# Performance work log

Measured on AMD Instinct MI355X. Metric: run time of the kernel, lower is better.

## Reference

```python
import jax, jax.numpy as jnp
import numpy as np

NM, ND = 50000, 50000          # mirna / disease node counts
DM, DD = 256, 256              # m_sim / d_sim feature dims
F = 64                         # feature_attn_size
E = 1600000                    # number of edges (avg degree 16)
N = NM + ND
SLOPE = 0.2                    # leaky_relu negative slope


def setup_inputs() -> dict:
    key = jax.random.key(0)
    k1, k2, k3, k4, k5, k6 = jax.random.split(key, 6)
    return {
        "m_sim": jax.random.normal(k1, (NM, DM), dtype=jnp.float32),
        "d_sim": jax.random.normal(k2, (ND, DD), dtype=jnp.float32),
        "Wm": jax.random.normal(k3, (F, DM), dtype=jnp.float32) / np.sqrt(DM).astype(np.float32),
        "Wd": jax.random.normal(k4, (F, DD), dtype=jnp.float32) / np.sqrt(DD).astype(np.float32),
        "src": jax.random.randint(k5, (E,), 0, N),
        "dst": jax.random.randint(k6, (E,), 0, N),
    }


def reference(m_sim, d_sim, Wm, Wd, src, dst):
    # node projection (dropout omitted: eval mode). mirna nodes first, then disease nodes.
    z = jnp.concatenate([m_sim @ Wm.T, d_sim @ Wd.T], axis=0)  # [N, F]

    # edge attention score: dot(z_src, z_dst) then leaky_relu
    z_src = z[src]                                             # [E, F] gather
    e = jnp.sum(z_src * z[dst], axis=1)                        # [E]
    e = jax.nn.leaky_relu(e, SLOPE)

    # segment softmax over incoming edges of each dst node (numerically stable)
    emax = jax.ops.segment_max(e, dst, num_segments=N)         # [N]
    emax = jnp.where(jnp.isfinite(emax), emax, 0.0)            # isolated nodes
    ex = jnp.exp(e - emax[dst])                                # [E]
    denom = jax.ops.segment_sum(ex, dst, num_segments=N)       # [N]
    alpha = ex / denom[dst]                                    # [E]

    # weighted aggregation + elu (isolated nodes get h=0, elu(0)=0)
    h = jax.ops.segment_sum(alpha[:, None] * z_src, dst, num_segments=N)  # [N, F]
    return jax.nn.elu(h)
```

## Files before the change

### kernel.cpp

```cpp
#include <hip/hip_runtime.h>
#include <math.h>

#define NM 50000
#define ND 50000
#define NN 100000
#define DK 256
#define F  64
#define SLOPE 0.2f

#define NBZ   782
#define NPROJ (NBZ * 2)

#define NBUCK 391
#define BCAP  8192
#define CH    4096

typedef short bf16x8 __attribute__((ext_vector_type(8)));
typedef float f32x4  __attribute__((ext_vector_type(4)));

__device__ __forceinline__ void gload_lds16(const void* g, void* l) {
    __builtin_amdgcn_global_load_lds((const __attribute__((address_space(1))) void*)g,
                                     (__attribute__((address_space(3))) void*)l, 16, 0, 0);
}

__device__ __forceinline__ void cvt8(const float4& a0, const float4& a1,
                                     bf16x8& hi, bf16x8& lo) {
    float v[8] = {a0.x, a0.y, a0.z, a0.w, a1.x, a1.y, a1.z, a1.w};
    #pragma unroll
    for (int e = 0; e < 8; ++e) {
        unsigned u  = __float_as_uint(v[e]);
        unsigned r  = u + 0x7FFF + ((u >> 16) & 1);
        unsigned short hb = (unsigned short)(r >> 16);
        float hf = __uint_as_float(((unsigned)hb) << 16);
        float lf = v[e] - hf;
        unsigned ul = __float_as_uint(lf);
        unsigned rl = ul + 0x7FFF + ((ul >> 16) & 1);
        hi[e] = (short)hb;
        lo[e] = (short)(rl >> 16);
    }
}

__global__ __launch_bounds__(256, 1) void fused1(const float* __restrict__ m_sim,
                                                 const float* __restrict__ d_sim,
                                                 const float* __restrict__ Wm,
                                                 const float* __restrict__ Wd,
                                                 float* __restrict__ z,
                                                 const int* __restrict__ src,
                                                 const int* __restrict__ dst,
                                                 int* __restrict__ pkb_g,
                                                 int* __restrict__ bcur,
                                                 int nchunks, int E) {
    __shared__ __align__(16) char smem[81920];
    int t = threadIdx.x;

    if ((int)blockIdx.x < nchunks) {
        int* cnt   = (int*)smem;
        int* scx   = cnt + 512;
        int* sp    = scx + 512;
        int* lcur  = sp + 256;
        int* gbase = lcur + 512;
        int* pkb_l = gbase + 512;
        int* bkt_l = pkb_l + CH;

        int base = blockIdx.x * CH;
        int chunkN = E - base; if (chunkN > CH) chunkN = CH;

        cnt[t] = 0; cnt[t + 256] = 0;
        __syncthreads();

        int ss[16], ds[16];
        #pragma unroll
        for (int e = 0; e < 16; ++e) {
            int k = base + e * 256 + t;
            if (e * 256 + t < chunkN) {
                ds[e] = dst[k];
                ss[e] = src[k];
                atomicAdd(&cnt[ds[e] >> 8], 1);
            }
        }
        __syncthreads();

        int a0 = cnt[2 * t], a1 = cnt[2 * t + 1];
        sp[t] = a0 + a1;
        __syncthreads();
        for (int off = 1; off < 256; off <<= 1) {
            int v = (t >= off) ? sp[t - off] : 0;
            __syncthreads();
            sp[t] += v;
            __syncthreads();
        }
        int pe = sp[t] - (a0 + a1);
        scx[2 * t]     = pe;
        scx[2 * t + 1] = pe + a0;
        lcur[2 * t]     = pe;
        lcur[2 * t + 1] = pe + a0;
        gbase[2 * t]     = atomicAdd(&bcur[2 * t],     a0);
        gbase[2 * t + 1] = atomicAdd(&bcur[2 * t + 1], a1);
        __syncthreads();

        #pragma unroll
        for (int e = 0; e < 16; ++e) {
            if (e * 256 + t < chunkN) {
                int b = ds[e] >> 8;
                int p = atomicAdd(&lcur[b], 1);
                pkb_l[p] = (ss[e] << 8) | (ds[e] & 255);
                bkt_l[p] = b;
            }
        }
        __syncthreads();

        for (int idx = t; idx < chunkN; idx += 256) {
            int b = bkt_l[idx];
            int g = b * BCAP + gbase[b] + (idx - scx[b]);
            pkb_g[g] = pkb_l[idx];
        }
        return;
    }

    float* As  = (float*)smem;
    short* Whi = (short*)(smem + 16384);
    short* Wlo = (short*)(smem + 49152);

    int bid  = blockIdx.x - nchunks;
    bool ism = bid < NBZ;
    const float* sim = ism ? m_sim : d_sim;
    const float* W   = ism ? Wm : Wd;
    int row0   = (ism ? bid : bid - NBZ) * 64;
    int nrows  = ism ? NM : ND;
    int zbase  = ism ? 0 : NM;

    int l = t & 63;
    int w = t >> 6;

    int srow = l >> 3;
    int ssw  = ((l & 7) ^ (srow & 7)) << 4;
    size_t aoff[2];
    #pragma unroll
    for (int q = 0; q < 2; ++q) {
        int r  = w * 16 + q * 8 + srow;
        int gr = row0 + r; if (gr > nrows - 1) gr = nrows - 1;
        aoff[q] = (size_t)gr * (DK * 4) + ssw;
    }
    #pragma unroll
    for (int q = 0; q < 2; ++q)
        gload_lds16((const char*)sim + aoff[q], (char*)As + (w * 16 + q * 8) * 128);

    {
        int r = t >> 2;
        int q = t & 3;
        const float4* wr = (const float4*)(W + (size_t)r * DK);
        #pragma unroll
        for (int i = 0; i < 8; ++i) {
            int ls = q * 8 + i;
            float4 b0 = wr[ls * 2], b1 = wr[ls * 2 + 1];
            bf16x8 hi, lo;
            cvt8(b0, b1, hi, lo);
            int ps = ls ^ (r & 7);
            *(bf16x8*)&Whi[r * 256 + ps * 8] = hi;
            *(bf16x8*)&Wlo[r * 256 + ps * 8] = lo;
        }
    }

    int frow = l & 15;
    int kg   = l >> 4;
    int s0   = kg * 2;
    int arow = w * 16 + frow;
    int aof0 = arow * 128 + (((s0    ) ^ (arow & 7)) << 4);
    int aof1 = arow * 128 + (((s0 + 1) ^ (arow & 7)) << 4);

    f32x4 acc[4];
    #pragma unroll
    for (int j = 0; j < 4; ++j) acc[j] = (f32x4){0.f, 0.f, 0.f, 0.f};

    const int NK = 8;

    #pragma unroll 1
    for (int step = 0; step < NK; ++step) {
        int cur = step & 1;
        __syncthreads();

        if (step + 1 < NK) {
            int koff = (step + 1) * 128;
            #pragma unroll
            for (int q = 0; q < 2; ++q)
                gload_lds16((const char*)sim + aoff[q] + koff,
                            (char*)As + (cur ^ 1) * 2048 * 4 + (w * 16 + q * 8) * 128);
        }

        float4 a0 = *(const float4*)((const char*)As + cur * 2048 * 4 + aof0);
        float4 a1 = *(const float4*)((const char*)As + cur * 2048 * 4 + aof1);
        bf16x8 ahi, alo;
        cvt8(a0, a1, ahi, alo);

        int ls = step * 4 + kg;
        #pragma unroll
        for (int j = 0; j < 4; ++j) {
            int wrow = j * 16 + frow;
            int ps = ls ^ (wrow & 7);
            bf16x8 bhi = *(const bf16x8*)&Whi[wrow * 256 + ps * 8];
            bf16x8 blo = *(const bf16x8*)&Wlo[wrow * 256 + ps * 8];
            acc[j] = __builtin_amdgcn_mfma_f32_16x16x32_bf16(ahi, bhi, acc[j], 0, 0, 0);
            acc[j] = __builtin_amdgcn_mfma_f32_16x16x32_bf16(ahi, blo, acc[j], 0, 0, 0);
            acc[j] = __builtin_amdgcn_mfma_f32_16x16x32_bf16(alo, bhi, acc[j], 0, 0, 0);
        }
    }

    #pragma unroll
    for (int j = 0; j < 4; ++j) {
        #pragma unroll
        for (int reg = 0; reg < 4; ++reg) {
            int r = row0 + w * 16 + kg * 4 + reg;
            if (r < nrows)
                z[(size_t)(zbase + r) * F + j * 16 + frow] = acc[j][reg];
        }
    }
}

__global__ __launch_bounds__(512) void scanBuck(const int* __restrict__ bcur,
                                                int* __restrict__ bbase) {
    __shared__ int sd[512];
    int t = threadIdx.x;
    int x = (t < NBUCK) ? bcur[t] : 0;
    sd[t] = x;
    __syncthreads();
    for (int off = 1; off < 512; off <<= 1) {
        int v = (t >= off) ? sd[t - off] : 0;
        __syncthreads();
        sd[t] += v;
        __syncthreads();
    }
    if (t < NBUCK) bbase[t] = sd[t] - x;
}

__global__ __launch_bounds__(256) void scatter3(const int* __restrict__ pkb_g,
                                                const int* __restrict__ bcur,
                                                const int* __restrict__ bbase,
                                                int* __restrict__ offs,
                                                int* __restrict__ csr) {
    __shared__ int dcnt[256], loc[256], lcur[256];
    int b = blockIdx.x;
    int t = threadIdx.x;
    int node0 = b << 8;
    int nbe  = bcur[b];
    int base = bbase[b];
    const int* pp = pkb_g + (size_t)b * BCAP;

    dcnt[t] = 0;
    __syncthreads();
    for (int i = t; i < nbe; i += 256)
        atomicAdd(&dcnt[pp[i] & 255], 1);
    __syncthreads();

    int x = dcnt[t];
    loc[t] = x;
    __syncthreads();
    for (int off = 1; off < 256; off <<= 1) {
        int v = (t >= off) ? loc[t - off] : 0;
        __syncthreads();
        loc[t] += v;
        __syncthreads();
    }
    int excl = loc[t] - x;
    int node = node0 + t;
    if (node < NN) offs[node] = base + excl;
    if (b == NBUCK - 1 && t == 0) offs[NN] = base + nbe;
    lcur[t] = base + excl;
    __syncthreads();

    for (int i = t; i < nbe; i += 256) {
        int pk = pp[i];
        int pos = atomicAdd(&lcur[pk & 255], 1);
        csr[pos] = pk >> 8;
    }
}

__global__ __launch_bounds__(256) void gat_kernel(const float* __restrict__ z,
                                                  const int* __restrict__ offs,
                                                  const int* __restrict__ csr_src,
                                                  float* __restrict__ out) {
    int tid  = threadIdx.x;
    int node = blockIdx.x * 4 + (tid >> 6);
    int lane = tid & 63;
    int g    = lane >> 4;
    int i    = lane & 15;
    int beg = offs[node];
    int end = offs[node + 1];

    float4 zd = *(const float4*)&z[(size_t)node * F + i * 4];

    float  m = -1e30f, ssum = 0.f;
    float4 h = {0.f, 0.f, 0.f, 0.f};

    for (int j = beg; j < end; j += 8) {
        int j0 = j + g, j1 = j + 4 + g;
        bool v0 = j0 < end, v1 = j1 < end;
        int s0 = csr_src[v0 ? j0 : beg];
        int s1 = csr_src[v1 ? j1 : beg];
        float4 a = *(const float4*)&z[(size_t)s0 * F + i * 4];
        float4 b = *(const float4*)&z[(size_t)s1 * F + i * 4];
        float p0 = a.x * zd.x + a.y * zd.y + a.z * zd.z + a.w * zd.w;
        float p1 = b.x * zd.x + b.y * zd.y + b.z * zd.z + b.w * zd.w;
        #pragma unroll
        for (int o = 1; o < 16; o <<= 1) {
            p0 += __shfl_xor(p0, o, 64);
            p1 += __shfl_xor(p1, o, 64);
        }
        float e0 = (p0 > 0.f) ? p0 : SLOPE * p0;
        float e1 = (p1 > 0.f) ? p1 : SLOPE * p1;
        e0 = v0 ? e0 : -1e30f;
        e1 = v1 ? e1 : -1e30f;
        float nm = fmaxf(m, fmaxf(e0, e1));
        float sc = __expf(m - nm);
        float ex0 = v0 ? __expf(e0 - nm) : 0.f;
        float ex1 = v1 ? __expf(e1 - nm) : 0.f;
        ssum = ssum * sc + ex0 + ex1;
        h.x = h.x * sc + ex0 * a.x + ex1 * b.x;
        h.y = h.y * sc + ex0 * a.y + ex1 * b.y;
        h.z = h.z * sc + ex0 * a.z + ex1 * b.z;
        h.w = h.w * sc + ex0 * a.w + ex1 * b.w;
        m = nm;
    }

    float M = fmaxf(m, __shfl_xor(m, 16, 64));
    M = fmaxf(M, __shfl_xor(M, 32, 64));
    float sc = __expf(m - M);
    float ss = ssum * sc;
    ss += __shfl_xor(ss, 16, 64);
    ss += __shfl_xor(ss, 32, 64);
    h.x *= sc; h.y *= sc; h.z *= sc; h.w *= sc;
    h.x += __shfl_xor(h.x, 16, 64); h.x += __shfl_xor(h.x, 32, 64);
    h.y += __shfl_xor(h.y, 16, 64); h.y += __shfl_xor(h.y, 32, 64);
    h.z += __shfl_xor(h.z, 16, 64); h.z += __shfl_xor(h.z, 32, 64);
    h.w += __shfl_xor(h.w, 16, 64); h.w += __shfl_xor(h.w, 32, 64);

    if (g == 0) {
        float rs = 1.0f / ss;
        bool has = end > beg;
        float4 o;
        o.x = has ? h.x * rs : 0.f;
        o.y = has ? h.y * rs : 0.f;
        o.z = has ? h.z * rs : 0.f;
        o.w = has ? h.w * rs : 0.f;
        o.x = (o.x > 0.f) ? o.x : (__expf(o.x) - 1.f);
        o.y = (o.y > 0.f) ? o.y : (__expf(o.y) - 1.f);
        o.z = (o.z > 0.f) ? o.z : (__expf(o.z) - 1.f);
        o.w = (o.w > 0.f) ? o.w : (__expf(o.w) - 1.f);
        *(float4*)&out[(size_t)node * F + i * 4] = o;
    }
}

extern "C" void kernel_launch(void* const* d_in, const int* in_sizes, int n_in,
                              void* d_out, int out_size, void* d_ws, size_t ws_size,
                              hipStream_t stream) {
    const float* m_sim = (const float*)d_in[0];
    const float* d_sim = (const float*)d_in[1];
    const float* Wm    = (const float*)d_in[2];
    const float* Wd    = (const float*)d_in[3];
    const int*   src   = (const int*)d_in[4];
    const int*   dst   = (const int*)d_in[5];
    int E = in_sizes[4];
    float* out = (float*)d_out;

    char* ws = (char*)d_ws;
    float* z      = (float*)ws; ws += (size_t)NN * F * 4;
    int*   offs   = (int*)ws;   ws += (size_t)(NN + 1) * 4;
    int*   bbase  = (int*)ws;   ws += 512 * 4;
    int*   bcur   = (int*)ws;   ws += 512 * 4;
    int*   csr    = (int*)ws;   ws += (size_t)E * 4;
    int*   pkb_g  = (int*)ws;   ws += (size_t)NBUCK * BCAP * 4;

    hipMemsetAsync(bcur, 0, 512 * 4, stream);

    int nchunks = (E + CH - 1) / CH;
    fused1<<<nchunks + NPROJ, 256, 0, stream>>>(m_sim, d_sim, Wm, Wd, z,
                                                src, dst, pkb_g, bcur, nchunks, E);
    scanBuck<<<1, 512, 0, stream>>>(bcur, bbase);
    scatter3<<<NBUCK, 256, 0, stream>>>(pkb_g, bcur, bbase, offs, csr);
    gat_kernel<<<NN / 4, 256, 0, stream>>>(z, offs, csr, out);
}
```

Measured before the change: 148.0 us.

## Widen fused1 to 512 threads, load A directly to registers, unroll GAT loop by 4

The fused bucketing/projection kernel moves to 512-thread blocks. Bucketing blocks now use a single 512-wide scan, and each projection block covers 128 rows while sharing one bf16 hi/lo copy of W. The projection no longer stages activations through LDS with async global-to-LDS loads. Each lane instead prefetches its own A fragments into registers two steps ahead, which drops per-step barriers but exposes raw global loads with no swizzled coalescing. The GAT kernel handles four neighbour edges per lane per iteration instead of two, raising memory-level parallelism for the random z gathers at the cost of more registers.

New measurement: 129.0 us. -12.8%, faster.

```diff
diff --git a/kernel.cpp b/kernel.cpp
--- a/kernel.cpp
+++ b/kernel.cpp
@@ -8,7 +8,7 @@
 #define F  64
 #define SLOPE 0.2f
 
-#define NBZ   782
+#define NBZ   391
 #define NPROJ (NBZ * 2)
 
 #define NBUCK 391
@@ -17,11 +17,6 @@
 
 typedef short bf16x8 __attribute__((ext_vector_type(8)));
 typedef float f32x4  __attribute__((ext_vector_type(4)));
-
-__device__ __forceinline__ void gload_lds16(const void* g, void* l) {
-    __builtin_amdgcn_global_load_lds((const __attribute__((address_space(1))) void*)g,
-                                     (__attribute__((address_space(3))) void*)l, 16, 0, 0);
-}
 
 __device__ __forceinline__ void cvt8(const float4& a0, const float4& a1,
                                      bf16x8& hi, bf16x8& lo) {
@@ -40,7 +35,7 @@
     }
 }
 
-__global__ __launch_bounds__(256, 1) void fused1(const float* __restrict__ m_sim,
+__global__ __launch_bounds__(512, 1) void fused1(const float* __restrict__ m_sim,
                                                  const float* __restrict__ d_sim,
                                                  const float* __restrict__ Wm,
                                                  const float* __restrict__ Wd,
@@ -50,14 +45,13 @@
                                                  int* __restrict__ pkb_g,
                                                  int* __restrict__ bcur,
                                                  int nchunks, int E) {
-    __shared__ __align__(16) char smem[81920];
+    __shared__ __align__(16) char smem[65536];
     int t = threadIdx.x;
 
     if ((int)blockIdx.x < nchunks) {
         int* cnt   = (int*)smem;
         int* scx   = cnt + 512;
-        int* sp    = scx + 512;
-        int* lcur  = sp + 256;
+        int* lcur  = scx + 512;
         int* gbase = lcur + 512;
         int* pkb_l = gbase + 512;
         int* bkt_l = pkb_l + CH;
@@ -65,14 +59,14 @@
         int base = blockIdx.x * CH;
         int chunkN = E - base; if (chunkN > CH) chunkN = CH;
 
-        cnt[t] = 0; cnt[t + 256] = 0;
-        __syncthreads();
-
-        int ss[16], ds[16];
-        #pragma unroll
-        for (int e = 0; e < 16; ++e) {
-            int k = base + e * 256 + t;
-            if (e * 256 + t < chunkN) {
+        cnt[t] = 0;
+        __syncthreads();
+
+        int ss[8], ds[8];
+        #pragma unroll
+        for (int e = 0; e < 8; ++e) {
+            int k = base + e * 512 + t;
+            if (e * 512 + t < chunkN) {
                 ds[e] = dst[k];
                 ss[e] = src[k];
                 atomicAdd(&cnt[ds[e] >> 8], 1);
@@ -80,27 +74,24 @@
         }
         __syncthreads();
 
-        int a0 = cnt[2 * t], a1 = cnt[2 * t + 1];
-        sp[t] = a0 + a1;
-        __syncthreads();
-        for (int off = 1; off < 256; off <<= 1) {
-            int v = (t >= off) ? sp[t - off] : 0;
+        int x = cnt[t];
+        scx[t] = x;
+        __syncthreads();
+        for (int off = 1; off < 512; off <<= 1) {
+            int v = (t >= off) ? scx[t - off] : 0;
             __syncthreads();
-            sp[t] += v;
+            scx[t] += v;
             __syncthreads();
         }
-        int pe = sp[t] - (a0 + a1);
-        scx[2 * t]     = pe;
-        scx[2 * t + 1] = pe + a0;
-        lcur[2 * t]     = pe;
-        lcur[2 * t + 1] = pe + a0;
-        gbase[2 * t]     = atomicAdd(&bcur[2 * t],     a0);
-        gbase[2 * t + 1] = atomicAdd(&bcur[2 * t + 1], a1);
-        __syncthreads();
-
-        #pragma unroll
-        for (int e = 0; e < 16; ++e) {
-            if (e * 256 + t < chunkN) {
+        int lexcl = scx[t] - x;
+        scx[t] = lexcl;
+        lcur[t] = lexcl;
+        gbase[t] = atomicAdd(&bcur[t], x);
+        __syncthreads();
+
+        #pragma unroll
+        for (int e = 0; e < 8; ++e) {
+            if (e * 512 + t < chunkN) {
                 int b = ds[e] >> 8;
                 int p = atomicAdd(&lcur[b], 1);
                 pkb_l[p] = (ss[e] << 8) | (ds[e] & 255);
@@ -109,7 +100,7 @@
         }
         __syncthreads();
 
-        for (int idx = t; idx < chunkN; idx += 256) {
+        for (int idx = t; idx < chunkN; idx += 512) {
             int b = bkt_l[idx];
             int g = b * BCAP + gbase[b] + (idx - scx[b]);
             pkb_g[g] = pkb_l[idx];
@@ -117,41 +108,35 @@
         return;
     }
 
-    float* As  = (float*)smem;
-    short* Whi = (short*)(smem + 16384);
-    short* Wlo = (short*)(smem + 49152);
+    short* Whi = (short*)smem;
+    short* Wlo = (short*)(smem + 32768);
 
     int bid  = blockIdx.x - nchunks;
     bool ism = bid < NBZ;
     const float* sim = ism ? m_sim : d_sim;
     const float* W   = ism ? Wm : Wd;
-    int row0   = (ism ? bid : bid - NBZ) * 64;
+    int row0   = (ism ? bid : bid - NBZ) * 128;
     int nrows  = ism ? NM : ND;
     int zbase  = ism ? 0 : NM;
 
     int l = t & 63;
     int w = t >> 6;
-
-    int srow = l >> 3;
-    int ssw  = ((l & 7) ^ (srow & 7)) << 4;
-    size_t aoff[2];
-    #pragma unroll
-    for (int q = 0; q < 2; ++q) {
-        int r  = w * 16 + q * 8 + srow;
-        int gr = row0 + r; if (gr > nrows - 1) gr = nrows - 1;
-        aoff[q] = (size_t)gr * (DK * 4) + ssw;
-    }
-    #pragma unroll
-    for (int q = 0; q < 2; ++q)
-        gload_lds16((const char*)sim + aoff[q], (char*)As + (w * 16 + q * 8) * 128);
+    int frow = l & 15;
+    int kg   = l >> 4;
+
+    int grow = row0 + w * 16 + frow; if (grow > nrows - 1) grow = nrows - 1;
+    const float4* ap = (const float4*)(sim + (size_t)grow * DK) + kg * 2;
+
+    float4 pa0 = ap[0], pa1 = ap[1];
+    float4 pb0 = ap[8], pb1 = ap[9];
 
     {
-        int r = t >> 2;
-        int q = t & 3;
+        int r = t >> 3;
+        int q = t & 7;
         const float4* wr = (const float4*)(W + (size_t)r * DK);
         #pragma unroll
-        for (int i = 0; i < 8; ++i) {
-            int ls = q * 8 + i;
+        for (int i = 0; i < 4; ++i) {
+            int ls = q * 4 + i;
             float4 b0 = wr[ls * 2], b1 = wr[ls * 2 + 1];
             bf16x8 hi, lo;
             cvt8(b0, b1, hi, lo);
@@ -160,37 +145,21 @@
             *(bf16x8*)&Wlo[r * 256 + ps * 8] = lo;
         }
     }
-
-    int frow = l & 15;
-    int kg   = l >> 4;
-    int s0   = kg * 2;
-    int arow = w * 16 + frow;
-    int aof0 = arow * 128 + (((s0    ) ^ (arow & 7)) << 4);
-    int aof1 = arow * 128 + (((s0 + 1) ^ (arow & 7)) << 4);
+    __syncthreads();
 
     f32x4 acc[4];
     #pragma unroll
     for (int j = 0; j < 4; ++j) acc[j] = (f32x4){0.f, 0.f, 0.f, 0.f};
 
-    const int NK = 8;
-
     #pragma unroll 1
-    for (int step = 0; step < NK; ++step) {
-        int cur = step & 1;
-        __syncthreads();
-
-        if (step + 1 < NK) {
-            int koff = (step + 1) * 128;
-            #pragma unroll
-            for (int q = 0; q < 2; ++q)
-                gload_lds16((const char*)sim + aoff[q] + koff,
-                            (char*)As + (cur ^ 1) * 2048 * 4 + (w * 16 + q * 8) * 128);
-        }
-
-        float4 a0 = *(const float4*)((const char*)As + cur * 2048 * 4 + aof0);
-        float4 a1 = *(const float4*)((const char*)As + cur * 2048 * 4 + aof1);
+    for (int step = 0; step < 8; ++step) {
         bf16x8 ahi, alo;
-        cvt8(a0, a1, ahi, alo);
+        cvt8(pa0, pa1, ahi, alo);
+        pa0 = pb0; pa1 = pb1;
+        if (step + 2 < 8) {
+            pb0 = ap[(step + 2) * 8];
+            pb1 = ap[(step + 2) * 8 + 1];
+        }
 
         int ls = step * 4 + kg;
         #pragma unroll
@@ -291,33 +260,42 @@
     float  m = -1e30f, ssum = 0.f;
     float4 h = {0.f, 0.f, 0.f, 0.f};
 
-    for (int j = beg; j < end; j += 8) {
-        int j0 = j + g, j1 = j + 4 + g;
-        bool v0 = j0 < end, v1 = j1 < end;
-        int s0 = csr_src[v0 ? j0 : beg];
-        int s1 = csr_src[v1 ? j1 : beg];
-        float4 a = *(const float4*)&z[(size_t)s0 * F + i * 4];
-        float4 b = *(const float4*)&z[(size_t)s1 * F + i * 4];
-        float p0 = a.x * zd.x + a.y * zd.y + a.z * zd.z + a.w * zd.w;
-        float p1 = b.x * zd.x + b.y * zd.y + b.z * zd.z + b.w * zd.w;
+    for (int j = beg; j < end; j += 16) {
+        int   idx[4];
+        bool  val[4];
+        float4 v[4];
+        float p[4], e[4], ex[4];
+        #pragma unroll
+        for (int k = 0; k < 4; ++k) {
+            int jj = j + k * 4 + g;
+            val[k] = jj < end;
+            idx[k] = csr_src[val[k] ? jj : beg];
+        }
+        #pragma unroll
+        for (int k = 0; k < 4; ++k)
+            v[k] = *(const float4*)&z[(size_t)idx[k] * F + i * 4];
+        #pragma unroll
+        for (int k = 0; k < 4; ++k)
+            p[k] = v[k].x * zd.x + v[k].y * zd.y + v[k].z * zd.z + v[k].w * zd.w;
         #pragma unroll
         for (int o = 1; o < 16; o <<= 1) {
-            p0 += __shfl_xor(p0, o, 64);
-            p1 += __shfl_xor(p1, o, 64);
-        }
-        float e0 = (p0 > 0.f) ? p0 : SLOPE * p0;
-        float e1 = (p1 > 0.f) ? p1 : SLOPE * p1;
-        e0 = v0 ? e0 : -1e30f;
-        e1 = v1 ? e1 : -1e30f;
-        float nm = fmaxf(m, fmaxf(e0, e1));
+            #pragma unroll
+            for (int k = 0; k < 4; ++k) p[k] += __shfl_xor(p[k], o, 64);
+        }
+        #pragma unroll
+        for (int k = 0; k < 4; ++k) {
+            float ek = (p[k] > 0.f) ? p[k] : SLOPE * p[k];
+            e[k] = val[k] ? ek : -1e30f;
+        }
+        float nm = fmaxf(m, fmaxf(fmaxf(e[0], e[1]), fmaxf(e[2], e[3])));
         float sc = __expf(m - nm);
-        float ex0 = v0 ? __expf(e0 - nm) : 0.f;
-        float ex1 = v1 ? __expf(e1 - nm) : 0.f;
-        ssum = ssum * sc + ex0 + ex1;
-        h.x = h.x * sc + ex0 * a.x + ex1 * b.x;
-        h.y = h.y * sc + ex0 * a.y + ex1 * b.y;
-        h.z = h.z * sc + ex0 * a.z + ex1 * b.z;
-        h.w = h.w * sc + ex0 * a.w + ex1 * b.w;
+        #pragma unroll
+        for (int k = 0; k < 4; ++k) ex[k] = val[k] ? __expf(e[k] - nm) : 0.f;
+        ssum = ssum * sc + ex[0] + ex[1] + ex[2] + ex[3];
+        h.x = h.x * sc + ex[0] * v[0].x + ex[1] * v[1].x + ex[2] * v[2].x + ex[3] * v[3].x;
+        h.y = h.y * sc + ex[0] * v[0].y + ex[1] * v[1].y + ex[2] * v[2].y + ex[3] * v[3].y;
+        h.z = h.z * sc + ex[0] * v[0].z + ex[1] * v[1].z + ex[2] * v[2].z + ex[3] * v[3].z;
+        h.w = h.w * sc + ex[0] * v[0].w + ex[1] * v[1].w + ex[2] * v[2].w + ex[3] * v[3].w;
         m = nm;
     }
 
@@ -372,7 +350,7 @@
     hipMemsetAsync(bcur, 0, 512 * 4, stream);
 
     int nchunks = (E + CH - 1) / CH;
-    fused1<<<nchunks + NPROJ, 256, 0, stream>>>(m_sim, d_sim, Wm, Wd, z,
+    fused1<<<nchunks + NPROJ, 512, 0, stream>>>(m_sim, d_sim, Wm, Wd, z,
                                                 src, dst, pkb_g, bcur, nchunks, E);
     scanBuck<<<1, 512, 0, stream>>>(bcur, bbase);
     scatter3<<<NBUCK, 256, 0, stream>>>(pkb_g, bcur, bbase, offs, csr);
```
